# Kernel tuning notes

Measured on AMD Instinct MI355X. Metric: run time of the kernel, lower is better.

Reference implementation:

```python
import jax, jax.numpy as jnp
import numpy as np

# Static config (must match init_kwargs)
IMG_H, IMG_W = 48, 160
BEV_H, BEV_W = 128, 128
X_MIN, X_MAX, Y_MIN, Y_MAX = -51.2, 51.2, -51.2, 51.2
RES_X = (X_MAX - X_MIN) / BEV_W
RES_Y = (Y_MAX - Y_MIN) / BEV_H
C, D, B = 128, 64, 2


def setup_inputs() -> dict:
    key = jax.random.key(0)
    k1, k2, k3, k4 = jax.random.split(key, 4)
    img_features = jax.random.normal(k1, (B, C, IMG_H, IMG_W), dtype=jnp.float32)
    # depth distribution per pixel (softmax over D, as a depth net would emit)
    depth_probs = jax.nn.softmax(jax.random.normal(k2, (B, D, IMG_H, IMG_W), dtype=jnp.float32), axis=1)
    # depth bin centers: 1m .. 60m
    depth_values = jnp.linspace(1.0, 60.0, D, dtype=jnp.float32)
    # realistic pinhole intrinsics (feature-map scale) with tiny per-cam jitter
    fx, fy, cx, cy = 120.0, 120.0, IMG_W / 2.0, IMG_H / 2.0
    K0 = jnp.array([[fx, 0.0, cx], [0.0, fy, cy], [0.0, 0.0, 1.0]], dtype=jnp.float32)
    K = K0[None] + 0.01 * jax.random.normal(k3, (B, 3, 3), dtype=jnp.float32) * jnp.array(
        [[1.0, 0.0, 1.0], [0.0, 1.0, 1.0], [0.0, 0.0, 0.0]], dtype=jnp.float32)
    # cam->lidar extrinsic: cam z (forward) -> lidar x, cam x -> -lidar y, cam y -> -lidar z
    R0 = jnp.array([[0.0, 0.0, 1.0], [-1.0, 0.0, 0.0], [0.0, -1.0, 0.0]], dtype=jnp.float32)
    t0 = jnp.array([1.5, 0.0, 1.8], dtype=jnp.float32)
    T0 = jnp.eye(4, dtype=jnp.float32).at[:3, :3].set(R0).at[:3, 3].set(t0)
    T = T0[None] + jnp.zeros((B, 4, 4), dtype=jnp.float32)
    T = T.at[:, :3, 3].add(0.05 * jax.random.normal(k4, (B, 3), dtype=jnp.float32))
    return {"img_features": img_features, "depth_probs": depth_probs,
            "depth_values": depth_values, "K": K, "T": T}


def _lss_forward(img_features, depth_probs, depth_values, K, T):
    Bn, Cn, H, W = img_features.shape
    Dn = depth_values.shape[0]
    # homogeneous pixel grid [H, W, 3]
    gx, gy = jnp.meshgrid(jnp.arange(W, dtype=jnp.float32),
                          jnp.arange(H, dtype=jnp.float32), indexing="xy")
    grid = jnp.stack([gx, gy, jnp.ones_like(gx)], axis=-1)
    # unproject: rays [B, H, W, 3]
    K_inv = jnp.linalg.inv(K)
    rays = jnp.einsum("bij,hwj->bhwi", K_inv, grid)
    # points in camera frame [B, D, H, W, 3]
    pts_cam = depth_values[None, :, None, None, None] * rays[:, None]
    # camera -> lidar
    pts = jnp.einsum("bij,bdhwj->bdhwi", T[:, :3, :3], pts_cam) + T[:, None, None, None, :3, 3]
    x, y, z = pts[..., 0], pts[..., 1], pts[..., 2]
    # torch .long() truncates toward zero -> astype int32 matches
    bx = ((x - X_MIN) / RES_X).astype(jnp.int32)
    by = ((y - Y_MIN) / RES_Y).astype(jnp.int32)
    valid = (bx >= 0) & (bx < BEV_W) & (by >= 0) & (by < BEV_H) & (z > 0)
    # depth-weighted features [B, D, H, W, C], masked instead of gathered
    weighted = jnp.einsum("bchw,bdhw->bdhwc", img_features, depth_probs)
    weighted = weighted * valid[..., None]
    idx = jnp.where(valid, by * BEV_W + bx, 0).reshape(Bn, -1)
    feats = weighted.reshape(Bn, -1, Cn)
    bev_flat = jax.vmap(lambda f, i: jax.ops.segment_sum(f, i, num_segments=BEV_H * BEV_W))(feats, idx)
    return bev_flat.reshape(Bn, BEV_H, BEV_W, Cn).transpose(0, 3, 1, 2)


def reference(img_features, depth_probs, depth_values, K, T):
    return _lss_forward(img_features, depth_probs, depth_values, K, T)
```

## Files before the change

kernel.cpp:

```cpp
#include <hip/hip_runtime.h>

constexpr int IMG_H = 48, IMG_W = 160;
constexpr int HW    = IMG_H * IMG_W;
constexpr int BEV_H = 128, BEV_W = 128;
constexpr int NCELL = BEV_H * BEV_W;
constexpr int C_DIM = 128, D_DIM = 64, B_DIM = 2;
constexpr int NCELL_TOT = B_DIM * NCELL;
constexpr int NPIX_TOT  = B_DIM * HW;
constexpr int NPTS      = NPIX_TOT * D_DIM;
constexpr int CHUNK = 64;
constexpr int NSHARD = 64;
constexpr float X_MIN = -51.2f, Y_MIN = -51.2f;
constexpr float RES_X = 102.4f / 128.0f;
constexpr float RES_Y = 102.4f / 128.0f;

constexpr size_t WS_IMG_T = 0;
constexpr size_t WS_DP_T  = WS_IMG_T + (size_t)B_DIM * HW * C_DIM;
constexpr size_t WS_HIST2 = WS_DP_T + (size_t)B_DIM * HW * D_DIM;
constexpr size_t WS_OUT_T = WS_HIST2 + (size_t)NSHARD * NCELL_TOT;
constexpr size_t WS_HIST  = WS_OUT_T + (size_t)NCELL_TOT * C_DIM;
constexpr size_t WS_OFFS  = WS_HIST + NCELL_TOT;
constexpr size_t WS_EKEY  = WS_OFFS + NCELL_TOT + 4;
constexpr size_t WS_EW16  = WS_EKEY + NPTS;

__device__ inline void make_ray(const float* __restrict__ K, int b, float gx, float gy,
                                float& rx, float& ry, float& rz) {
    const float* Kb = K + b * 9;
    const float a00 = Kb[0], a01 = Kb[1], a02 = Kb[2];
    const float a10 = Kb[3], a11 = Kb[4], a12 = Kb[5];
    const float a20 = Kb[6], a21 = Kb[7], a22 = Kb[8];
    const float det = a00 * (a11 * a22 - a12 * a21)
                    - a01 * (a10 * a22 - a12 * a20)
                    + a02 * (a10 * a21 - a11 * a20);
    const float inv = 1.0f / det;
    const float i00 =  (a11 * a22 - a12 * a21) * inv;
    const float i01 = -(a01 * a22 - a02 * a21) * inv;
    const float i02 =  (a01 * a12 - a02 * a11) * inv;
    const float i10 = -(a10 * a22 - a12 * a20) * inv;
    const float i11 =  (a00 * a22 - a02 * a20) * inv;
    const float i12 = -(a00 * a12 - a02 * a10) * inv;
    const float i20 =  (a10 * a21 - a11 * a20) * inv;
    const float i21 = -(a00 * a21 - a01 * a20) * inv;
    const float i22 =  (a00 * a11 - a01 * a10) * inv;
    rx = i00 * gx + i01 * gy + i02;
    ry = i10 * gx + i11 * gy + i12;
    rz = i20 * gx + i21 * gy + i22;
}

__device__ inline int gcell_ray(int b, int pix, int d,
                                const float* __restrict__ dv,
                                const float* __restrict__ K,
                                const float* __restrict__ T) {
    const int h = pix / IMG_W, w = pix % IMG_W;
    float rx, ry, rz;
    make_ray(K, b, (float)w, (float)h, rx, ry, rz);
    const float* Tb = T + b * 16;
    const float dep = dv[d];
    const float px = dep * rx, py = dep * ry, pz = dep * rz;
    const float x = Tb[0] * px + Tb[1] * py + Tb[2]  * pz + Tb[3];
    const float y = Tb[4] * px + Tb[5] * py + Tb[6]  * pz + Tb[7];
    const float z = Tb[8] * px + Tb[9] * py + Tb[10] * pz + Tb[11];
    const int bx = (int)((x - X_MIN) / RES_X);
    const int by = (int)((y - Y_MIN) / RES_Y);
    const bool valid = (bx >= 0) && (bx < BEV_W) && (by >= 0) && (by < BEV_H) && (z > 0.0f);
    return valid ? (b * NCELL + by * BEV_W + bx) : -1;
}

struct RunInfo { int leader_idx; bool is_tail; };
__device__ inline RunInfo wave_runs_d(int gcell, int lane) {
    const int left = __shfl_up(gcell, 1);
    const bool is_leader = (lane == 0) || (left != gcell);
    const unsigned long long lmask = __ballot(is_leader);
    const unsigned long long below =
        lmask & ((lane == 63) ? ~0ULL : ((1ULL << (lane + 1)) - 1ULL));
    RunInfo r;
    r.leader_idx = 63 - __clzll((long long)below);
    r.is_tail = (lane == 63) || ((lmask >> (lane + 1)) & 1ULL);
    return r;
}

__device__ inline int shard_of(int pix) { return (pix ^ (pix >> 6)) & (NSHARD - 1); }

constexpr int NB_IMG = (HW / 32) * (C_DIM / 32) * B_DIM;
constexpr int NB_DP  = (HW / 32) * (D_DIM / 32) * B_DIM;
constexpr int NB_CNT = NPTS / 256;
__global__ __launch_bounds__(256) void k_prep(const float* __restrict__ img,
                                              const float* __restrict__ dp,
                                              const float* __restrict__ dv,
                                              const float* __restrict__ K,
                                              const float* __restrict__ T,
                                              float* __restrict__ img_t,
                                              float* __restrict__ dp_t,
                                              int* __restrict__ hist2) {
    int bid = blockIdx.x;
    if (bid < NB_IMG + NB_DP) {
        const float* src; float* dst; int rows;
        if (bid < NB_IMG) { src = img; dst = img_t; rows = C_DIM; }
        else              { bid -= NB_IMG; src = dp; dst = dp_t; rows = D_DIM; }
        const int tiles_c = rows / 32;
        const int b = bid / ((HW / 32) * tiles_c);
        const int r = bid % ((HW / 32) * tiles_c);
        const int ctile = r / (HW / 32), ptile = r % (HW / 32);
        __shared__ float tile[32][33];
        const int tx = threadIdx.x & 31, ty = threadIdx.x >> 5;
        const int pix0 = ptile * 32, c0 = ctile * 32;
        #pragma unroll
        for (int j = 0; j < 32; j += 8)
            tile[ty + j][tx] = src[((size_t)(b * rows + c0 + ty + j)) * HW + pix0 + tx];
        __syncthreads();
        #pragma unroll
        for (int j = 0; j < 32; j += 8)
            dst[((size_t)(b * HW + pix0 + ty + j)) * rows + c0 + tx] = tile[tx][ty + j];
    } else {
        const int tid = (bid - NB_IMG - NB_DP) * 256 + threadIdx.x;
        const int lane = threadIdx.x & 63;
        const int wid = tid >> 6;
        const int b = wid / HW, pix = wid % HW;
        const int gcell = gcell_ray(b, pix, lane, dv, K, T);
        const RunInfo ri = wave_runs_d(gcell, lane);
        if (ri.is_tail && gcell >= 0)
            atomicAdd(&hist2[(size_t)shard_of(pix) * NCELL_TOT + gcell], 1);
    }
}

__global__ __launch_bounds__(256) void k_reduce(const int* __restrict__ hist2,
                                                int* __restrict__ hist) {
    const int cell = blockIdx.x * 256 + threadIdx.x;
    int s = 0;
    #pragma unroll
    for (int sh = 0; sh < NSHARD; ++sh)
        s += hist2[(size_t)sh * NCELL_TOT + cell];
    hist[cell] = s;
}

__global__ __launch_bounds__(1024) void k_scan(const int* __restrict__ hist,
                                               int* __restrict__ offs) {
    __shared__ int lds[1024];
    const int t = threadIdx.x;
    int h[32];
    int s = 0;
    const int base = t * 32;
    #pragma unroll
    for (int k = 0; k < 32; ++k) { h[k] = hist[base + k]; s += h[k]; }
    lds[t] = s;
    __syncthreads();
    for (int off = 1; off < 1024; off <<= 1) {
        int v = (t >= off) ? lds[t - off] : 0;
        __syncthreads();
        lds[t] += v;
        __syncthreads();
    }
    int run = lds[t] - s;
    #pragma unroll
    for (int k = 0; k < 32; ++k) {
        offs[base + k] = run;
        run += h[k];
    }
    if (t == 1023) offs[NCELL_TOT] = lds[1023];
}

__global__ __launch_bounds__(256) void k_shardbase(int* __restrict__ hist2,
                                                   const int* __restrict__ offs) {
    const int cell = blockIdx.x * 256 + threadIdx.x;
    int run = offs[cell];
    #pragma unroll
    for (int sh = 0; sh < NSHARD; ++sh) {
        const size_t idx = (size_t)sh * NCELL_TOT + cell;
        const int cnt = hist2[idx];
        hist2[idx] = run;
        run += cnt;
    }
}

__global__ __launch_bounds__(256) void k_fill(const float* __restrict__ dp_t,
                                              const float* __restrict__ dv,
                                              const float* __restrict__ K,
                                              const float* __restrict__ T,
                                              int* __restrict__ cursor2,
                                              int* __restrict__ ekey,
                                              unsigned short* __restrict__ ew16) {
    const int tid = blockIdx.x * 256 + threadIdx.x;
    const int lane = threadIdx.x & 63;
    const int wid = tid >> 6;
    const int b = wid / HW, pix = wid % HW;
    const int gcell = gcell_ray(b, pix, lane, dv, K, T);
    const RunInfo ri = wave_runs_d(gcell, lane);
    const float p = dp_t[((size_t)(b * HW + pix)) * D_DIM + lane];
    float val = p;
    #pragma unroll
    for (int dlt = 1; dlt < 64; dlt <<= 1) {
        const float up = __shfl_up(val, dlt);
        val = (lane - dlt >= ri.leader_idx) ? val + up : val;
    }
    if (ri.is_tail && gcell >= 0) {
        const int slot = atomicAdd(&cursor2[(size_t)shard_of(pix) * NCELL_TOT + gcell], 1);
        ekey[slot] = (gcell << 13) | pix;
        ew16[slot] = (unsigned short)__float2uint_rn(fminf(val * 65535.0f, 65535.0f));
    }
}

__global__ __launch_bounds__(64) void k_gather(
    const float* __restrict__ img_t,
    const int* __restrict__ offs,
    const int* __restrict__ ekey,
    const unsigned short* __restrict__ ew16,
    float* __restrict__ out_t)
{
    const int total = offs[NCELL_TOT];
    const int base = blockIdx.x * CHUNK;
    if (base >= total) return;

    __shared__ int   s_key[CHUNK];
    __shared__ float s_w[CHUNK];
    {
        const int i = threadIdx.x;
        const int idx = min(base + i, total - 1);
        s_key[i] = ekey[idx];
        s_w[i]   = (base + i < total) ? (float)ew16[base + i] * (1.0f / 65535.0f)
                                      : 0.0f;
    }
    __syncthreads();

    const int c2 = threadIdx.x * 2;
    int prev = s_key[0] >> 13;
    float2 acc = make_float2(0.0f, 0.0f);
    #pragma unroll 8
    for (int k = 0; k < CHUNK; ++k) {
        const int key = s_key[k];
        const float wgt = s_w[k];
        const int gcell = key >> 13;
        const int pix = key & 8191;
        const int b = gcell >> 14;
        const float2 v = *reinterpret_cast<const float2*>(
            &img_t[((size_t)(b * HW + pix)) * C_DIM + c2]);
        if (gcell != prev) {
            float* o = &out_t[(size_t)prev * C_DIM + c2];
            atomicAdd(o, acc.x);
            atomicAdd(o + 1, acc.y);
            acc = make_float2(0.0f, 0.0f);
            prev = gcell;
        }
        acc.x = fmaf(v.x, wgt, acc.x);
        acc.y = fmaf(v.y, wgt, acc.y);
    }
    float* o = &out_t[(size_t)prev * C_DIM + c2];
    atomicAdd(o, acc.x);
    atomicAdd(o + 1, acc.y);
}

__global__ __launch_bounds__(256) void k_untranspose(const float* __restrict__ out_t,
                                                     float* __restrict__ out) {
    __shared__ float tile[32][33];
    const int b = blockIdx.z;
    const int tx = threadIdx.x, ty = threadIdx.y;
    const int cell0 = blockIdx.x * 32, c0 = blockIdx.y * 32;
    const float* src = out_t + (size_t)b * NCELL * C_DIM;
    #pragma unroll
    for (int j = 0; j < 32; j += 8)
        tile[ty + j][tx] = src[((size_t)(cell0 + ty + j)) * C_DIM + c0 + tx];
    __syncthreads();
    #pragma unroll
    for (int j = 0; j < 32; j += 8)
        out[((size_t)(b * C_DIM + c0 + ty + j)) * NCELL + cell0 + tx] = tile[tx][ty + j];
}

extern "C" void kernel_launch(void* const* d_in, const int* in_sizes, int n_in,
                              void* d_out, int out_size, void* d_ws, size_t ws_size,
                              hipStream_t stream) {
    const float* img = (const float*)d_in[0];
    const float* dp  = (const float*)d_in[1];
    const float* dv  = (const float*)d_in[2];
    const float* K   = (const float*)d_in[3];
    const float* T   = (const float*)d_in[4];
    float* out = (float*)d_out;

    float* ws_f   = (float*)d_ws;
    float* img_t  = ws_f + WS_IMG_T;
    float* dp_t   = ws_f + WS_DP_T;
    int*   hist2  = (int*)d_ws + WS_HIST2;
    float* out_t  = ws_f + WS_OUT_T;
    int*   hist   = (int*)d_ws + WS_HIST;
    int*   offs   = (int*)d_ws + WS_OFFS;
    int*   ekey   = (int*)d_ws + WS_EKEY;
    unsigned short* ew16 = (unsigned short*)((int*)d_ws + WS_EW16);

    hipMemsetAsync(hist2, 0,
                   ((size_t)NSHARD * NCELL_TOT + (size_t)NCELL_TOT * C_DIM) * sizeof(int),
                   stream);

    k_prep<<<NB_IMG + NB_DP + NB_CNT, 256, 0, stream>>>(img, dp, dv, K, T,
                                                        img_t, dp_t, hist2);
    k_reduce<<<NCELL_TOT / 256, 256, 0, stream>>>(hist2, hist);
    k_scan<<<1, 1024, 0, stream>>>(hist, offs);
    k_shardbase<<<NCELL_TOT / 256, 256, 0, stream>>>(hist2, offs);
    k_fill<<<NPTS / 256, 256, 0, stream>>>(dp_t, dv, K, T, hist2, ekey, ew16);
    k_gather<<<NPTS / CHUNK, 64, 0, stream>>>(img_t, offs, ekey, ew16, out_t);
    k_untranspose<<<dim3(NCELL / 32, C_DIM / 32, B_DIM), dim3(32, 8), 0, stream>>>(
        out_t, out);
}
```

Before: 172.5 us.

## Transpose shard histogram layout, pack entries as uint2, map batches to XCD halves

Stores the per-shard histogram cell-major so reduce and shardbase read contiguous rows, and vectorizes those reads with int4. Fill entries become a single packed uint2 holding key and full-precision weight instead of split key and 16-bit weight arrays. Gather blocks are remapped so batch 0 chunks go to four XCDs and batch 1 chunks to the other four, aiming to keep each batch's image features in a shared L2. The cost is doubled entry storage traffic, and per-cell rows in k_reduce/k_shardbase are strided across threads, which may coalesce poorly.

Measured after the change: 334.2 us. 1.94x slower.

```diff
diff --git a/kernel.cpp b/kernel.cpp
--- a/kernel.cpp
+++ b/kernel.cpp
@@ -17,11 +17,10 @@
 constexpr size_t WS_IMG_T = 0;
 constexpr size_t WS_DP_T  = WS_IMG_T + (size_t)B_DIM * HW * C_DIM;
 constexpr size_t WS_HIST2 = WS_DP_T + (size_t)B_DIM * HW * D_DIM;
-constexpr size_t WS_OUT_T = WS_HIST2 + (size_t)NSHARD * NCELL_TOT;
+constexpr size_t WS_OUT_T = WS_HIST2 + (size_t)NCELL_TOT * NSHARD;
 constexpr size_t WS_HIST  = WS_OUT_T + (size_t)NCELL_TOT * C_DIM;
 constexpr size_t WS_OFFS  = WS_HIST + NCELL_TOT;
-constexpr size_t WS_EKEY  = WS_OFFS + NCELL_TOT + 4;
-constexpr size_t WS_EW16  = WS_EKEY + NPTS;
+constexpr size_t WS_ENT   = WS_OFFS + NCELL_TOT + 4;
 
 __device__ inline void make_ray(const float* __restrict__ K, int b, float gx, float gy,
                                 float& rx, float& ry, float& rz) {
@@ -119,17 +118,20 @@
         const int gcell = gcell_ray(b, pix, lane, dv, K, T);
         const RunInfo ri = wave_runs_d(gcell, lane);
         if (ri.is_tail && gcell >= 0)
-            atomicAdd(&hist2[(size_t)shard_of(pix) * NCELL_TOT + gcell], 1);
+            atomicAdd(&hist2[(size_t)gcell * NSHARD + shard_of(pix)], 1);
     }
 }
 
 __global__ __launch_bounds__(256) void k_reduce(const int* __restrict__ hist2,
                                                 int* __restrict__ hist) {
     const int cell = blockIdx.x * 256 + threadIdx.x;
+    const int4* row = reinterpret_cast<const int4*>(hist2 + (size_t)cell * NSHARD);
     int s = 0;
     #pragma unroll
-    for (int sh = 0; sh < NSHARD; ++sh)
-        s += hist2[(size_t)sh * NCELL_TOT + cell];
+    for (int k = 0; k < NSHARD / 4; ++k) {
+        const int4 v = row[k];
+        s += v.x + v.y + v.z + v.w;
+    }
     hist[cell] = s;
 }
 
@@ -140,8 +142,13 @@
     int h[32];
     int s = 0;
     const int base = t * 32;
-    #pragma unroll
-    for (int k = 0; k < 32; ++k) { h[k] = hist[base + k]; s += h[k]; }
+    const int4* hv = reinterpret_cast<const int4*>(hist + base);
+    #pragma unroll
+    for (int k = 0; k < 8; ++k) {
+        const int4 v = hv[k];
+        h[4 * k] = v.x; h[4 * k + 1] = v.y; h[4 * k + 2] = v.z; h[4 * k + 3] = v.w;
+        s += v.x + v.y + v.z + v.w;
+    }
     lds[t] = s;
     __syncthreads();
     for (int off = 1; off < 1024; off <<= 1) {
@@ -162,12 +169,12 @@
 __global__ __launch_bounds__(256) void k_shardbase(int* __restrict__ hist2,
                                                    const int* __restrict__ offs) {
     const int cell = blockIdx.x * 256 + threadIdx.x;
+    int* row = hist2 + (size_t)cell * NSHARD;
     int run = offs[cell];
     #pragma unroll
     for (int sh = 0; sh < NSHARD; ++sh) {
-        const size_t idx = (size_t)sh * NCELL_TOT + cell;
-        const int cnt = hist2[idx];
-        hist2[idx] = run;
+        const int cnt = row[sh];
+        row[sh] = run;
         run += cnt;
     }
 }
@@ -177,8 +184,7 @@
                                               const float* __restrict__ K,
                                               const float* __restrict__ T,
                                               int* __restrict__ cursor2,
-                                              int* __restrict__ ekey,
-                                              unsigned short* __restrict__ ew16) {
+                                              uint2* __restrict__ ent) {
     const int tid = blockIdx.x * 256 + threadIdx.x;
     const int lane = threadIdx.x & 63;
     const int wid = tid >> 6;
@@ -193,31 +199,42 @@
         val = (lane - dlt >= ri.leader_idx) ? val + up : val;
     }
     if (ri.is_tail && gcell >= 0) {
-        const int slot = atomicAdd(&cursor2[(size_t)shard_of(pix) * NCELL_TOT + gcell], 1);
-        ekey[slot] = (gcell << 13) | pix;
-        ew16[slot] = (unsigned short)__float2uint_rn(fminf(val * 65535.0f, 65535.0f));
+        const int slot = atomicAdd(&cursor2[(size_t)gcell * NSHARD + shard_of(pix)], 1);
+        ent[slot] = make_uint2((unsigned)((gcell << 13) | pix), __float_as_uint(val));
     }
 }
 
 __global__ __launch_bounds__(64) void k_gather(
     const float* __restrict__ img_t,
     const int* __restrict__ offs,
-    const int* __restrict__ ekey,
-    const unsigned short* __restrict__ ew16,
+    const uint2* __restrict__ ent,
     float* __restrict__ out_t)
 {
     const int total = offs[NCELL_TOT];
-    const int base = blockIdx.x * CHUNK;
-    if (base >= total) return;
+    const int n0 = offs[NCELL];
+    const int nch0 = (n0 + CHUNK - 1) / CHUNK;
+    const int nch_tot = (total + CHUNK - 1) / CHUNK;
+
+    const int xcd = blockIdx.x & 7;
+    const int slot = blockIdx.x >> 3;
+    int chunk;
+    if (xcd < 4) {
+        chunk = slot * 4 + xcd;
+        if (chunk >= nch0) return;
+    } else {
+        chunk = nch0 + slot * 4 + (xcd - 4);
+        if (chunk >= nch_tot) return;
+    }
+    const int base = chunk * CHUNK;
 
     __shared__ int   s_key[CHUNK];
     __shared__ float s_w[CHUNK];
     {
         const int i = threadIdx.x;
         const int idx = min(base + i, total - 1);
-        s_key[i] = ekey[idx];
-        s_w[i]   = (base + i < total) ? (float)ew16[base + i] * (1.0f / 65535.0f)
-                                      : 0.0f;
+        const uint2 e = ent[idx];
+        s_key[i] = (int)e.x;
+        s_w[i]   = (base + i < total) ? __uint_as_float(e.y) : 0.0f;
     }
     __syncthreads();
 
@@ -281,11 +298,10 @@
     float* out_t  = ws_f + WS_OUT_T;
     int*   hist   = (int*)d_ws + WS_HIST;
     int*   offs   = (int*)d_ws + WS_OFFS;
-    int*   ekey   = (int*)d_ws + WS_EKEY;
-    unsigned short* ew16 = (unsigned short*)((int*)d_ws + WS_EW16);
+    uint2* ent    = (uint2*)((int*)d_ws + WS_ENT);
 
     hipMemsetAsync(hist2, 0,
-                   ((size_t)NSHARD * NCELL_TOT + (size_t)NCELL_TOT * C_DIM) * sizeof(int),
+                   ((size_t)NCELL_TOT * NSHARD + (size_t)NCELL_TOT * C_DIM) * sizeof(int),
                    stream);
 
     k_prep<<<NB_IMG + NB_DP + NB_CNT, 256, 0, stream>>>(img, dp, dv, K, T,
@@ -293,8 +309,8 @@
     k_reduce<<<NCELL_TOT / 256, 256, 0, stream>>>(hist2, hist);
     k_scan<<<1, 1024, 0, stream>>>(hist, offs);
     k_shardbase<<<NCELL_TOT / 256, 256, 0, stream>>>(hist2, offs);
-    k_fill<<<NPTS / 256, 256, 0, stream>>>(dp_t, dv, K, T, hist2, ekey, ew16);
-    k_gather<<<NPTS / CHUNK, 64, 0, stream>>>(img_t, offs, ekey, ew16, out_t);
+    k_fill<<<NPTS / 256, 256, 0, stream>>>(dp_t, dv, K, T, hist2, ent);
+    k_gather<<<NPTS / CHUNK, 64, 0, stream>>>(img_t, offs, ent, out_t);
     k_untranspose<<<dim3(NCELL / 32, C_DIM / 32, B_DIM), dim3(32, 8), 0, stream>>>(
         out_t, out);
 }
```
